# Kernel tuning notes

Measured on AMD Instinct MI355X. Metric: run time of the kernel, lower is better.

## Reference

```python
import jax, jax.numpy as jnp
import numpy as np

B, S, D, H = 4, 4096, 1024, 64

def setup_inputs() -> dict:
    key = jax.random.key(0)
    k1, k2, k3, k4 = jax.random.split(key, 4)
    inp = {
        'input': jax.random.normal(k1, (B, S, D), dtype=jnp.float32),
        'Wq': jax.random.normal(k2, (D, H), dtype=jnp.float32) * (D ** -0.5),
        'Wk': jax.random.normal(k3, (D, H), dtype=jnp.float32) * (D ** -0.5),
        'Wv': jax.random.normal(k4, (D, H), dtype=jnp.float32) * (D ** -0.5),
    }
    return inp

def reference(input, Wq, Wk, Wv):
    # Projections: [B,S,D] @ [D,H] -> [B,S,H]
    q = input @ Wq
    k = input @ Wk
    v = input @ Wv
    head_size = Wq.shape[-1]
    # Scaled scores: [B,S,S]
    scores = jnp.einsum('bqh,bkh->bqk', q, k) * (head_size ** -0.5)
    seq_len = input.shape[1]
    causal = jnp.tril(jnp.ones((seq_len, seq_len), dtype=bool))
    masked = jnp.where(causal, scores, -jnp.inf)
    weights = jax.nn.softmax(masked, axis=-1)
    # dropout p=0.0 -> identity
    return jnp.einsum('bqk,bkh->bqh', weights, v)
```

## Files before the change

### kernel.cpp

```cpp
#include <hip/hip_runtime.h>

#define NS 8

typedef __attribute__((ext_vector_type(8))) short sh8;
typedef __attribute__((ext_vector_type(4))) short sh4;
typedef __attribute__((ext_vector_type(4))) float f4;

#define QSCALE 0.18033688011112042f

typedef const __attribute__((address_space(1))) unsigned int* gas_t;
typedef __attribute__((address_space(3))) unsigned int* las_t;
#define GLD16(g, l) __builtin_amdgcn_global_load_lds((gas_t)(g), (las_t)(l), 16, 0, 0)

static __device__ __forceinline__ unsigned short f2bf(float f) {
  unsigned u = __builtin_bit_cast(unsigned, f);
  u += 0x7fffu + ((u >> 16) & 1u);
  return (unsigned short)(u >> 16);
}
static __device__ __forceinline__ float bf2f(unsigned short s) {
  unsigned u = ((unsigned)s) << 16;
  return __builtin_bit_cast(float, u);
}

__global__ __launch_bounds__(256) void wt_kernel(const float* __restrict__ Wq,
                                                 const float* __restrict__ Wk,
                                                 const float* __restrict__ Wv,
                                                 unsigned short* __restrict__ Wt) {
  __shared__ float tile[64 * 65];
  int widx = blockIdx.x >> 4, kt = blockIdx.x & 15;
  const float* W = widx == 0 ? Wq : (widx == 1 ? Wk : Wv);
  int t = threadIdx.x;
  {
    int kl = t >> 2, seg = (t & 3) * 16;
    const float* src = W + (size_t)(kt * 64 + kl) * 64 + seg;
#pragma unroll
    for (int j = 0; j < 16; ++j) tile[kl * 65 + seg + j] = src[j];
  }
  __syncthreads();
  {
    int nl = t >> 2, ks = (t & 3) * 16;
    unsigned short* dst = Wt + (size_t)(widx * 64 + nl) * 1024 + kt * 64 + ks;
#pragma unroll
    for (int j = 0; j < 16; ++j) dst[j] = f2bf(tile[(ks + j) * 65 + nl]);
  }
}

__global__ __launch_bounds__(256, 4) void proj_kernel(const float* __restrict__ in,
                                                      const unsigned short* __restrict__ Wt,
                                                      unsigned short* __restrict__ Qg,
                                                      unsigned short* __restrict__ Kg,
                                                      unsigned short* __restrict__ Vtg) {
  __shared__ __align__(16) char lds[32768];
  int t = threadIdx.x;
  int w = t >> 6, lane = t & 63, q = lane >> 4, l15 = lane & 15;
  int m0 = blockIdx.x * 32;

  int mt_s = w >> 1, i_s = w & 1;
  const float* ga = in + (size_t)(m0 + mt_s * 16 + l15) * 1024 + q * 8 + i_s * 4;
  const unsigned short* gb = Wt + (size_t)(w * 48 + l15) * 1024 + q * 8;

  f4 acc[2][3];
  f4 z = {0.f, 0.f, 0.f, 0.f};
#pragma unroll
  for (int mt = 0; mt < 2; ++mt)
#pragma unroll
    for (int nt = 0; nt < 3; ++nt) acc[mt][nt] = z;

#define STAGE(kt, buf)                                                        \
  {                                                                           \
    int k0 = (kt) * 32;                                                       \
    char* base = lds + (buf) * 16384;                                         \
    GLD16(ga + k0, base + w * 1024);                                          \
    GLD16(gb + k0, base + 4096 + (w * 3 + 0) * 1024);                         \
    GLD16(gb + 16384 + k0, base + 4096 + (w * 3 + 1) * 1024);                 \
    GLD16(gb + 32768 + k0, base + 4096 + (w * 3 + 2) * 1024);                 \
  }

  STAGE(0, 0);
  for (int kt = 0; kt < 32; ++kt) {
    int cur = kt & 1;
    __syncthreads();
    if (kt + 1 < 32) STAGE(kt + 1, cur ^ 1);

    const f4* Af = (const f4*)(lds + cur * 16384);
    f4 lo0 = Af[0 * 64 + lane], hi0 = Af[1 * 64 + lane];
    f4 lo1 = Af[2 * 64 + lane], hi1 = Af[3 * 64 + lane];
    sh8 a0, a1;
#pragma unroll
    for (int j = 0; j < 4; ++j) {
      a0[j] = (short)f2bf(lo0[j]); a0[4 + j] = (short)f2bf(hi0[j]);
      a1[j] = (short)f2bf(lo1[j]); a1[4 + j] = (short)f2bf(hi1[j]);
    }
    const sh8* Bf = (const sh8*)(lds + cur * 16384 + 4096);
#pragma unroll
    for (int nt = 0; nt < 3; ++nt) {
      sh8 bf = Bf[(w * 3 + nt) * 64 + lane];
      acc[0][nt] = __builtin_amdgcn_mfma_f32_16x16x32_bf16(a0, bf, acc[0][nt], 0, 0, 0);
      acc[1][nt] = __builtin_amdgcn_mfma_f32_16x16x32_bf16(a1, bf, acc[1][nt], 0, 0, 0);
    }
  }
#undef STAGE

  float* vred = (float*)lds;
#pragma unroll
  for (int nt = 0; nt < 3; ++nt) {
    int band = w * 3 + nt;
#pragma unroll
    for (int mt = 0; mt < 2; ++mt)
#pragma unroll
      for (int r = 0; r < 4; ++r) {
        int row = mt * 16 + q * 4 + r;
        float v = acc[mt][nt][r];
        if (band < 4) {
          Qg[(size_t)(m0 + row) * 64 + band * 16 + l15] = f2bf(v * QSCALE);
        } else if (band < 8) {
          Kg[(size_t)(m0 + row) * 64 + (band - 4) * 16 + l15] = f2bf(v);
        } else {
          vred[row * 69 + (band - 8) * 16 + l15] = v;
        }
      }
  }
  __syncthreads();
  {
    int h = t >> 2, sl = (t & 3) * 8;
    int bb = m0 >> 12, s0 = m0 & 4095;
    sh8 vv;
#pragma unroll
    for (int j = 0; j < 8; ++j) vv[j] = (short)f2bf(vred[(sl + j) * 69 + h]);
    *(sh8*)&Vtg[(((size_t)(bb * 64 + h)) << 12) + s0 + sl] = vv;
  }
}

__global__ __launch_bounds__(256, 4) void attn_split(const unsigned short* __restrict__ Qg,
                                                     const unsigned short* __restrict__ Kg,
                                                     const unsigned short* __restrict__ Vtg,
                                                     unsigned short* __restrict__ Opart,
                                                     float* __restrict__ Lpart) {
  __shared__ unsigned short Ks[64 * 72];
  __shared__ unsigned short Vs[64 * 72];
  __shared__ unsigned short Pw[4 * 16 * 72];
  int t = threadIdx.x;
  int b = blockIdx.y;
  int qt = 63 - (int)(blockIdx.x >> 3);
  int sp = blockIdx.x & 7;
  int wave = t >> 6, lane = t & 63, quad = lane >> 4, l15 = lane & 15;
  unsigned short* Pws = Pw + wave * 16 * 72;

  int qrow0 = qt * 64 + wave * 16;
  size_t pbase = ((size_t)sp * 4 + b) * 4096;

  int nkt = qt + 1;
  int chunk = (nkt + NS - 1) / NS;
  int t0 = sp * chunk, t1 = min(nkt, t0 + chunk);
  if (t0 >= t1) {
#pragma unroll
    for (int r = 0; r < 4; ++r) {
      size_t row = pbase + qrow0 + quad * 4 + r;
#pragma unroll
      for (int ht = 0; ht < 4; ++ht) Opart[row * 64 + ht * 16 + l15] = 0;
      if (l15 == 0) Lpart[row] = 0.f;
    }
    return;
  }

  sh8 qa[2];
#pragma unroll
  for (int ks = 0; ks < 2; ++ks)
    qa[ks] = *(const sh8*)&Qg[(size_t)((b << 12) + qrow0 + l15) * 64 + ks * 32 + quad * 8];

  sh8 ones;
#pragma unroll
  for (int j = 0; j < 8; ++j) ones[j] = (short)0x3F80;

  f4 o[5];
  f4 z = {0.f, 0.f, 0.f, 0.f};
#pragma unroll
  for (int ht = 0; ht < 5; ++ht) o[ht] = z;

  int r0 = t >> 3, o0 = (t & 7) * 8;
  int r1 = (t + 256) >> 3, o1 = ((t + 256) & 7) * 8;
  const unsigned short* kg0 = Kg + (size_t)((b << 12) + r0) * 64 + o0;
  const unsigned short* kg1 = Kg + (size_t)((b << 12) + r1) * 64 + o1;
  const unsigned short* vg0 = Vtg + (((size_t)(b * 64 + r0)) << 12) + o0;
  const unsigned short* vg1 = Vtg + (((size_t)(b * 64 + r1)) << 12) + o1;

  sh8 kr0, kr1, vr0, vr1;
  {
    size_t ko = (size_t)t0 * 64 * 64;
    kr0 = *(const sh8*)(kg0 + ko); kr1 = *(const sh8*)(kg1 + ko);
    vr0 = *(const sh8*)(vg0 + t0 * 64); vr1 = *(const sh8*)(vg1 + t0 * 64);
  }

  for (int kt = t0; kt < t1; ++kt) {
    __syncthreads();
    *(sh8*)&Ks[r0 * 72 + o0] = kr0;
    *(sh8*)&Ks[r1 * 72 + o1] = kr1;
    *(sh8*)&Vs[r0 * 72 + o0] = vr0;
    *(sh8*)&Vs[r1 * 72 + o1] = vr1;
    if (kt + 1 < t1) {
      size_t ko = (size_t)(kt + 1) * 64 * 64;
      kr0 = *(const sh8*)(kg0 + ko); kr1 = *(const sh8*)(kg1 + ko);
      vr0 = *(const sh8*)(vg0 + (kt + 1) * 64); vr1 = *(const sh8*)(vg1 + (kt + 1) * 64);
    }
    __syncthreads();

    f4 st[4];
#pragma unroll
    for (int nt = 0; nt < 4; ++nt) st[nt] = z;
#pragma unroll
    for (int ks = 0; ks < 2; ++ks) {
#pragma unroll
      for (int nt = 0; nt < 4; ++nt) {
        sh8 kb = *(const sh8*)&Ks[(nt * 16 + l15) * 72 + ks * 32 + quad * 8];
        st[nt] = __builtin_amdgcn_mfma_f32_16x16x32_bf16(kb, qa[ks], st[nt], 0, 0, 0);
      }
    }

    if (kt == nkt - 1) {
      int qrow = qrow0 + l15;
#pragma unroll
      for (int nt = 0; nt < 4; ++nt) {
        int key0 = kt * 64 + nt * 16 + quad * 4;
#pragma unroll
        for (int r = 0; r < 4; ++r)
          if (key0 + r > qrow) st[nt][r] = -__builtin_inff();
      }
    }

#pragma unroll
    for (int nt = 0; nt < 4; ++nt) {
      sh4 pk;
#pragma unroll
      for (int r = 0; r < 4; ++r) pk[r] = (short)f2bf(exp2f(st[nt][r]));
      *(sh4*)&Pws[l15 * 72 + nt * 16 + quad * 4] = pk;
    }
    asm volatile("s_waitcnt lgkmcnt(0)" ::: "memory");

#pragma unroll
    for (int ks = 0; ks < 2; ++ks) {
      sh8 pa = *(const sh8*)&Pws[l15 * 72 + ks * 32 + quad * 8];
#pragma unroll
      for (int ht = 0; ht < 4; ++ht) {
        sh8 vb = *(const sh8*)&Vs[(ht * 16 + l15) * 72 + ks * 32 + quad * 8];
        o[ht] = __builtin_amdgcn_mfma_f32_16x16x32_bf16(pa, vb, o[ht], 0, 0, 0);
      }
      o[4] = __builtin_amdgcn_mfma_f32_16x16x32_bf16(pa, ones, o[4], 0, 0, 0);
    }
  }

#pragma unroll
  for (int r = 0; r < 4; ++r) {
    size_t row = pbase + qrow0 + quad * 4 + r;
#pragma unroll
    for (int ht = 0; ht < 4; ++ht)
      Opart[row * 64 + ht * 16 + l15] = f2bf(o[ht][r]);
    if (l15 == 0) Lpart[row] = o[4][r];
  }
}

__global__ __launch_bounds__(256) void attn_combine(const unsigned short* __restrict__ Opart,
                                                    const float* __restrict__ Lpart,
                                                    float* __restrict__ out) {
  int t = threadIdx.x;
  int rg = blockIdx.x * 4 + (t >> 6);
  int lane = t & 63;
  float acc = 0.f, L = 0.f;
#pragma unroll
  for (int s = 0; s < NS; ++s) {
    L += Lpart[(size_t)s * 16384 + rg];
    acc += bf2f(Opart[((size_t)s * 16384 + rg) * 64 + lane]);
  }
  out[(size_t)rg * 64 + lane] = acc / L;
}

extern "C" void kernel_launch(void* const* d_in, const int* in_sizes, int n_in,
                              void* d_out, int out_size, void* d_ws, size_t ws_size,
                              hipStream_t stream) {
  const float* in = (const float*)d_in[0];
  const float* Wq = (const float*)d_in[1];
  const float* Wk = (const float*)d_in[2];
  const float* Wv = (const float*)d_in[3];
  float* out = (float*)d_out;

  char* ws = (char*)d_ws;
  unsigned short* Wt    = (unsigned short*)ws;
  unsigned short* Qg    = (unsigned short*)(ws + 393216);
  unsigned short* Kg    = (unsigned short*)(ws + 2490368);
  unsigned short* Vtg   = (unsigned short*)(ws + 4587520);
  unsigned short* Opart = (unsigned short*)(ws + 6684672);
  float*          Lpart = (float*)(ws + 23461888);

  hipLaunchKernelGGL(wt_kernel, dim3(48), dim3(256), 0, stream, Wq, Wk, Wv, Wt);
  hipLaunchKernelGGL(proj_kernel, dim3(512), dim3(256), 0, stream, in, Wt, Qg, Kg, Vtg);
  hipLaunchKernelGGL(attn_split, dim3(64 * NS, 4), dim3(256), 0, stream,
                     Qg, Kg, Vtg, Opart, Lpart);
  hipLaunchKernelGGL(attn_combine, dim3(4096), dim3(256), 0, stream,
                     Opart, Lpart, out);
}
```

Measured before the change: 159.4 us.

## Split projection K-dimension across blocks and process two query tiles per attention block

The projection GEMM is split in two along K, with each half written as bf16 partials and summed in a new proj_combine kernel that also produces Q, K and the transposed V. Attention blocks now handle two 64-row query tiles over a shared K/V tile load, which halves K/V staging per query and halves the grid. The aim is more parallelism in the projection and more K/V reuse in attention. The cost is an extra kernel launch, an extra round-trip of partials through memory, bf16 rounding of partial sums, and fewer attention blocks.

New measurement: 180.8 us. 1.13x slower.

```diff
diff --git a/kernel.cpp b/kernel.cpp
--- a/kernel.cpp
+++ b/kernel.cpp
@@ -47,17 +47,17 @@
 
 __global__ __launch_bounds__(256, 4) void proj_kernel(const float* __restrict__ in,
                                                       const unsigned short* __restrict__ Wt,
-                                                      unsigned short* __restrict__ Qg,
-                                                      unsigned short* __restrict__ Kg,
-                                                      unsigned short* __restrict__ Vtg) {
+                                                      unsigned short* __restrict__ Pp) {
   __shared__ __align__(16) char lds[32768];
   int t = threadIdx.x;
   int w = t >> 6, lane = t & 63, q = lane >> 4, l15 = lane & 15;
-  int m0 = blockIdx.x * 32;
+  int m0 = (blockIdx.x >> 1) * 32;
+  int ksp = blockIdx.x & 1;
+  int kbase = ksp * 512;
 
   int mt_s = w >> 1, i_s = w & 1;
-  const float* ga = in + (size_t)(m0 + mt_s * 16 + l15) * 1024 + q * 8 + i_s * 4;
-  const unsigned short* gb = Wt + (size_t)(w * 48 + l15) * 1024 + q * 8;
+  const float* ga = in + (size_t)(m0 + mt_s * 16 + l15) * 1024 + kbase + q * 8 + i_s * 4;
+  const unsigned short* gb = Wt + (size_t)(w * 48 + l15) * 1024 + kbase + q * 8;
 
   f4 acc[2][3];
   f4 z = {0.f, 0.f, 0.f, 0.f};
@@ -77,10 +77,10 @@
   }
 
   STAGE(0, 0);
-  for (int kt = 0; kt < 32; ++kt) {
+  for (int kt = 0; kt < 16; ++kt) {
     int cur = kt & 1;
     __syncthreads();
-    if (kt + 1 < 32) STAGE(kt + 1, cur ^ 1);
+    if (kt + 1 < 16) STAGE(kt + 1, cur ^ 1);
 
     const f4* Af = (const f4*)(lds + cur * 16384);
     f4 lo0 = Af[0 * 64 + lane], hi0 = Af[1 * 64 + lane];
@@ -101,7 +101,6 @@
   }
 #undef STAGE
 
-  float* vred = (float*)lds;
 #pragma unroll
   for (int nt = 0; nt < 3; ++nt) {
     int band = w * 3 + nt;
@@ -110,24 +109,46 @@
 #pragma unroll
       for (int r = 0; r < 4; ++r) {
         int row = mt * 16 + q * 4 + r;
-        float v = acc[mt][nt][r];
-        if (band < 4) {
-          Qg[(size_t)(m0 + row) * 64 + band * 16 + l15] = f2bf(v * QSCALE);
-        } else if (band < 8) {
-          Kg[(size_t)(m0 + row) * 64 + (band - 4) * 16 + l15] = f2bf(v);
-        } else {
-          vred[row * 69 + (band - 8) * 16 + l15] = v;
-        }
+        Pp[((size_t)ksp * 16384 + m0 + row) * 192 + band * 16 + l15] = f2bf(acc[mt][nt][r]);
+      }
+  }
+}
+
+__global__ __launch_bounds__(256) void proj_combine(const unsigned short* __restrict__ Pp,
+                                                    unsigned short* __restrict__ Qg,
+                                                    unsigned short* __restrict__ Kg,
+                                                    unsigned short* __restrict__ Vtg) {
+  __shared__ unsigned short vtile[64 * 72];
+  int t = threadIdx.x;
+  int m0 = blockIdx.x * 64;
+  int row = t >> 2, cg = t & 3;
+  {
+    const sh8* p0 = (const sh8*)(Pp + (size_t)(m0 + row) * 192 + cg * 48);
+    const sh8* p1 = (const sh8*)(Pp + ((size_t)16384 + m0 + row) * 192 + cg * 48);
+    sh8 a0[6], a1[6];
+#pragma unroll
+    for (int i = 0; i < 6; ++i) { a0[i] = p0[i]; a1[i] = p1[i]; }
+#pragma unroll
+    for (int i = 0; i < 6; ++i)
+#pragma unroll
+      for (int j = 0; j < 8; ++j) {
+        int c = cg * 48 + i * 8 + j;
+        float v = bf2f((unsigned short)a0[i][j]) + bf2f((unsigned short)a1[i][j]);
+        if (c < 64)       Qg[(size_t)(m0 + row) * 64 + c] = f2bf(v * QSCALE);
+        else if (c < 128) Kg[(size_t)(m0 + row) * 64 + (c - 64)] = f2bf(v);
+        else              vtile[row * 72 + (c - 128)] = f2bf(v);
       }
   }
   __syncthreads();
   {
-    int h = t >> 2, sl = (t & 3) * 8;
+    int h = t >> 2, ss = (t & 3) * 16;
     int bb = m0 >> 12, s0 = m0 & 4095;
-    sh8 vv;
-#pragma unroll
-    for (int j = 0; j < 8; ++j) vv[j] = (short)f2bf(vred[(sl + j) * 69 + h]);
-    *(sh8*)&Vtg[(((size_t)(bb * 64 + h)) << 12) + s0 + sl] = vv;
+    unsigned short tmp[16];
+#pragma unroll
+    for (int j = 0; j < 16; ++j) tmp[j] = vtile[(ss + j) * 72 + h];
+    unsigned short* dst = Vtg + (((size_t)(bb * 64 + h)) << 12) + s0 + ss;
+    *(sh8*)dst = *(sh8*)tmp;
+    *(sh8*)(dst + 8) = *(sh8*)(tmp + 8);
   }
 }
 
@@ -141,41 +162,47 @@
   __shared__ unsigned short Pw[4 * 16 * 72];
   int t = threadIdx.x;
   int b = blockIdx.y;
-  int qt = 63 - (int)(blockIdx.x >> 3);
+  int qt = 31 - (int)(blockIdx.x >> 3);
   int sp = blockIdx.x & 7;
   int wave = t >> 6, lane = t & 63, quad = lane >> 4, l15 = lane & 15;
   unsigned short* Pws = Pw + wave * 16 * 72;
 
-  int qrow0 = qt * 64 + wave * 16;
+  int qrow0[2] = {qt * 128 + wave * 16, qt * 128 + 64 + wave * 16};
   size_t pbase = ((size_t)sp * 4 + b) * 4096;
 
-  int nkt = qt + 1;
+  int nkt = 2 * qt + 2;
   int chunk = (nkt + NS - 1) / NS;
   int t0 = sp * chunk, t1 = min(nkt, t0 + chunk);
   if (t0 >= t1) {
 #pragma unroll
-    for (int r = 0; r < 4; ++r) {
-      size_t row = pbase + qrow0 + quad * 4 + r;
-#pragma unroll
-      for (int ht = 0; ht < 4; ++ht) Opart[row * 64 + ht * 16 + l15] = 0;
-      if (l15 == 0) Lpart[row] = 0.f;
-    }
+    for (int s = 0; s < 2; ++s)
+#pragma unroll
+      for (int r = 0; r < 4; ++r) {
+        size_t row = pbase + qrow0[s] + quad * 4 + r;
+#pragma unroll
+        for (int ht = 0; ht < 4; ++ht) Opart[row * 64 + ht * 16 + l15] = 0;
+        if (l15 == 0) Lpart[row] = 0.f;
+      }
     return;
   }
 
-  sh8 qa[2];
-#pragma unroll
-  for (int ks = 0; ks < 2; ++ks)
-    qa[ks] = *(const sh8*)&Qg[(size_t)((b << 12) + qrow0 + l15) * 64 + ks * 32 + quad * 8];
+  sh8 qa[2][2];
+#pragma unroll
+  for (int s = 0; s < 2; ++s)
+#pragma unroll
+    for (int ks = 0; ks < 2; ++ks)
+      qa[s][ks] = *(const sh8*)&Qg[(size_t)((b << 12) + qrow0[s] + l15) * 64 + ks * 32 + quad * 8];
 
   sh8 ones;
 #pragma unroll
   for (int j = 0; j < 8; ++j) ones[j] = (short)0x3F80;
 
-  f4 o[5];
+  f4 o[2][5];
   f4 z = {0.f, 0.f, 0.f, 0.f};
 #pragma unroll
-  for (int ht = 0; ht < 5; ++ht) o[ht] = z;
+  for (int s = 0; s < 2; ++s)
+#pragma unroll
+    for (int ht = 0; ht < 5; ++ht) o[s][ht] = z;
 
   int r0 = t >> 3, o0 = (t & 7) * 8;
   int r1 = (t + 256) >> 3, o1 = ((t + 256) & 7) * 8;
@@ -204,58 +231,65 @@
     }
     __syncthreads();
 
-    f4 st[4];
-#pragma unroll
-    for (int nt = 0; nt < 4; ++nt) st[nt] = z;
-#pragma unroll
-    for (int ks = 0; ks < 2; ++ks) {
+#pragma unroll
+    for (int s = 0; s < 2; ++s) {
+      if (kt > 2 * qt + s) continue;
+
+      f4 st[4];
+#pragma unroll
+      for (int nt = 0; nt < 4; ++nt) st[nt] = z;
+#pragma unroll
+      for (int ks = 0; ks < 2; ++ks) {
+#pragma unroll
+        for (int nt = 0; nt < 4; ++nt) {
+          sh8 kb = *(const sh8*)&Ks[(nt * 16 + l15) * 72 + ks * 32 + quad * 8];
+          st[nt] = __builtin_amdgcn_mfma_f32_16x16x32_bf16(kb, qa[s][ks], st[nt], 0, 0, 0);
+        }
+      }
+
+      if (kt == 2 * qt + s) {
+        int qrow = qrow0[s] + l15;
+#pragma unroll
+        for (int nt = 0; nt < 4; ++nt) {
+          int key0 = kt * 64 + nt * 16 + quad * 4;
+#pragma unroll
+          for (int r = 0; r < 4; ++r)
+            if (key0 + r > qrow) st[nt][r] = -__builtin_inff();
+        }
+      }
+
 #pragma unroll
       for (int nt = 0; nt < 4; ++nt) {
-        sh8 kb = *(const sh8*)&Ks[(nt * 16 + l15) * 72 + ks * 32 + quad * 8];
-        st[nt] = __builtin_amdgcn_mfma_f32_16x16x32_bf16(kb, qa[ks], st[nt], 0, 0, 0);
-      }
-    }
-
-    if (kt == nkt - 1) {
-      int qrow = qrow0 + l15;
-#pragma unroll
-      for (int nt = 0; nt < 4; ++nt) {
-        int key0 = kt * 64 + nt * 16 + quad * 4;
-#pragma unroll
-        for (int r = 0; r < 4; ++r)
-          if (key0 + r > qrow) st[nt][r] = -__builtin_inff();
-      }
-    }
-
-#pragma unroll
-    for (int nt = 0; nt < 4; ++nt) {
-      sh4 pk;
-#pragma unroll
-      for (int r = 0; r < 4; ++r) pk[r] = (short)f2bf(exp2f(st[nt][r]));
-      *(sh4*)&Pws[l15 * 72 + nt * 16 + quad * 4] = pk;
-    }
-    asm volatile("s_waitcnt lgkmcnt(0)" ::: "memory");
-
-#pragma unroll
-    for (int ks = 0; ks < 2; ++ks) {
-      sh8 pa = *(const sh8*)&Pws[l15 * 72 + ks * 32 + quad * 8];
-#pragma unroll
-      for (int ht = 0; ht < 4; ++ht) {
-        sh8 vb = *(const sh8*)&Vs[(ht * 16 + l15) * 72 + ks * 32 + quad * 8];
-        o[ht] = __builtin_amdgcn_mfma_f32_16x16x32_bf16(pa, vb, o[ht], 0, 0, 0);
-      }
-      o[4] = __builtin_amdgcn_mfma_f32_16x16x32_bf16(pa, ones, o[4], 0, 0, 0);
-    }
-  }
-
-#pragma unroll
-  for (int r = 0; r < 4; ++r) {
-    size_t row = pbase + qrow0 + quad * 4 + r;
-#pragma unroll
-    for (int ht = 0; ht < 4; ++ht)
-      Opart[row * 64 + ht * 16 + l15] = f2bf(o[ht][r]);
-    if (l15 == 0) Lpart[row] = o[4][r];
-  }
+        sh4 pk;
+#pragma unroll
+        for (int r = 0; r < 4; ++r) pk[r] = (short)f2bf(exp2f(st[nt][r]));
+        *(sh4*)&Pws[l15 * 72 + nt * 16 + quad * 4] = pk;
+      }
+      asm volatile("s_waitcnt lgkmcnt(0)" ::: "memory");
+
+#pragma unroll
+      for (int ks = 0; ks < 2; ++ks) {
+        sh8 pa = *(const sh8*)&Pws[l15 * 72 + ks * 32 + quad * 8];
+#pragma unroll
+        for (int ht = 0; ht < 4; ++ht) {
+          sh8 vb = *(const sh8*)&Vs[(ht * 16 + l15) * 72 + ks * 32 + quad * 8];
+          o[s][ht] = __builtin_amdgcn_mfma_f32_16x16x32_bf16(pa, vb, o[s][ht], 0, 0, 0);
+        }
+        o[s][4] = __builtin_amdgcn_mfma_f32_16x16x32_bf16(pa, ones, o[s][4], 0, 0, 0);
+      }
+    }
+  }
+
+#pragma unroll
+  for (int s = 0; s < 2; ++s)
+#pragma unroll
+    for (int r = 0; r < 4; ++r) {
+      size_t row = pbase + qrow0[s] + quad * 4 + r;
+#pragma unroll
+      for (int ht = 0; ht < 4; ++ht)
+        Opart[row * 64 + ht * 16 + l15] = f2bf(o[s][ht][r]);
+      if (l15 == 0) Lpart[row] = o[s][4][r];
+    }
 }
 
 __global__ __launch_bounds__(256) void attn_combine(const unsigned short* __restrict__ Opart,
@@ -284,15 +318,17 @@
 
   char* ws = (char*)d_ws;
   unsigned short* Wt    = (unsigned short*)ws;
-  unsigned short* Qg    = (unsigned short*)(ws + 393216);
-  unsigned short* Kg    = (unsigned short*)(ws + 2490368);
-  unsigned short* Vtg   = (unsigned short*)(ws + 4587520);
-  unsigned short* Opart = (unsigned short*)(ws + 6684672);
-  float*          Lpart = (float*)(ws + 23461888);
+  unsigned short* Pp    = (unsigned short*)(ws + 393216);
+  unsigned short* Qg    = (unsigned short*)(ws + 12976128);
+  unsigned short* Kg    = (unsigned short*)(ws + 15073280);
+  unsigned short* Vtg   = (unsigned short*)(ws + 17170432);
+  unsigned short* Opart = (unsigned short*)(ws + 19267584);
+  float*          Lpart = (float*)(ws + 36044800);
 
   hipLaunchKernelGGL(wt_kernel, dim3(48), dim3(256), 0, stream, Wq, Wk, Wv, Wt);
-  hipLaunchKernelGGL(proj_kernel, dim3(512), dim3(256), 0, stream, in, Wt, Qg, Kg, Vtg);
-  hipLaunchKernelGGL(attn_split, dim3(64 * NS, 4), dim3(256), 0, stream,
+  hipLaunchKernelGGL(proj_kernel, dim3(1024), dim3(256), 0, stream, in, Wt, Pp);
+  hipLaunchKernelGGL(proj_combine, dim3(256), dim3(256), 0, stream, Pp, Qg, Kg, Vtg);
+  hipLaunchKernelGGL(attn_split, dim3(32 * NS, 4), dim3(256), 0, stream,
                      Qg, Kg, Vtg, Opart, Lpart);
   hipLaunchKernelGGL(attn_combine, dim3(4096), dim3(256), 0, stream,
                      Opart, Lpart, out);
```
